# Optimization experiments

Measured on AMD Instinct MI355X. Metric: run time of the kernel, lower is better.

## Reference

```python
import jax, jax.numpy as jnp
import numpy as np
from jax import lax

# Model dims (mamba_ssm defaults: d_state=16, d_conv=4, expand=2, dt_rank=ceil(d_model/16))
V = 16384       # vocab_size
D = 1024        # embedding_dim / d_model
C_CLS = 128     # num_CLS_classes
D_INNER = 2 * D # expand * d_model = 2048
N = 16          # d_state
K = 4           # d_conv
DT_RANK = (D + 15) // 16  # 64
B, L = 4, 512


def setup_inputs() -> dict:
    key = jax.random.key(0)
    ks = jax.random.split(key, 12)
    s = 0.02
    tokens = jax.random.randint(ks[0], (B, L), 0, V, dtype=jnp.int64)
    embedding = jax.random.normal(ks[1], (V, D), jnp.float32) * s
    in_proj_w = jax.random.normal(ks[2], (2 * D_INNER, D), jnp.float32) * s
    conv_w = jax.random.normal(ks[3], (D_INNER, 1, K), jnp.float32) * 0.1
    conv_b = jnp.zeros((D_INNER,), jnp.float32)
    x_proj_w = jax.random.normal(ks[4], (DT_RANK + 2 * N, D_INNER), jnp.float32) * s
    dt_proj_w = jax.random.normal(ks[5], (D_INNER, DT_RANK), jnp.float32) * s
    dt_proj_b = jax.random.uniform(ks[6], (D_INNER,), jnp.float32, -4.0, -2.0)  # softplus -> small dt
    A_log = jnp.log(jnp.broadcast_to(jnp.arange(1, N + 1, dtype=jnp.float32), (D_INNER, N)))
    D_param = jnp.ones((D_INNER,), jnp.float32)
    out_proj_w = jax.random.normal(ks[7], (D, D_INNER), jnp.float32) * s
    recon_w = jax.random.normal(ks[8], (V, D), jnp.float32) * s
    cls_w = jax.random.normal(ks[9], (C_CLS, D), jnp.float32) * s
    return dict(tokens=tokens, embedding=embedding, in_proj_w=in_proj_w,
                conv_w=conv_w, conv_b=conv_b, x_proj_w=x_proj_w,
                dt_proj_w=dt_proj_w, dt_proj_b=dt_proj_b, A_log=A_log,
                D_param=D_param, out_proj_w=out_proj_w, recon_w=recon_w, cls_w=cls_w)


def _mamba(h, in_proj_w, conv_w, conv_b, x_proj_w, dt_proj_w, dt_proj_b, A_log, D_param, out_proj_w):
    # h: (B, L, D)
    xz = jnp.einsum('bld,ed->ble', h, in_proj_w)          # (B, L, 2*D_INNER)
    x, z = jnp.split(xz, 2, axis=-1)                      # each (B, L, D_INNER)
    # causal depthwise conv1d along L
    xt = jnp.swapaxes(x, 1, 2)                            # (B, D_INNER, L)
    xt = lax.conv_general_dilated(xt, conv_w, window_strides=(1,),
                                  padding=[(K - 1, 0)],
                                  feature_group_count=D_INNER,
                                  dimension_numbers=('NCH', 'OIH', 'NCH'))
    xt = xt + conv_b[None, :, None]
    x = jax.nn.silu(jnp.swapaxes(xt, 1, 2))               # (B, L, D_INNER)
    # input-dependent dt, B, C
    x_dbl = jnp.einsum('bld,ed->ble', x, x_proj_w)        # (B, L, DT_RANK+2N)
    dt, Bm, Cm = jnp.split(x_dbl, [DT_RANK, DT_RANK + N], axis=-1)
    delta = jax.nn.softplus(jnp.einsum('blr,dr->bld', dt, dt_proj_w) + dt_proj_b)  # (B,L,D_INNER)
    A = -jnp.exp(A_log)                                   # (D_INNER, N)
    dA = jnp.exp(delta[..., None] * A)                    # (B,L,D_INNER,N)
    dBx = delta[..., None] * Bm[:, :, None, :] * x[..., None]  # (B,L,D_INNER,N)
    # selective scan over time (sequential recurrence)
    dA_t = jnp.swapaxes(dA, 0, 1)                         # (L,B,D_INNER,N)
    dBx_t = jnp.swapaxes(dBx, 0, 1)
    C_t = jnp.swapaxes(Cm, 0, 1)                          # (L,B,N)
    def step(hc, inp):
        a, bx, c = inp
        hc = a * hc + bx                                  # (B,D_INNER,N)
        y = jnp.einsum('bdn,bn->bd', hc, c)
        return hc, y
    h0 = jnp.zeros((x.shape[0], D_INNER, N), x.dtype)
    _, ys = lax.scan(step, h0, (dA_t, dBx_t, C_t))
    y = jnp.swapaxes(ys, 0, 1) + x * D_param              # (B,L,D_INNER)
    y = y * jax.nn.silu(z)
    return jnp.einsum('ble,de->bld', y, out_proj_w)       # (B,L,D)


def reference(tokens, embedding, in_proj_w, conv_w, conv_b, x_proj_w,
              dt_proj_w, dt_proj_b, A_log, D_param, out_proj_w, recon_w, cls_w):
    h = embedding[tokens]                                 # (B,L,D)
    h = _mamba(h, in_proj_w, conv_w, conv_b, x_proj_w, dt_proj_w, dt_proj_b,
               A_log, D_param, out_proj_w)
    recon = jnp.einsum('bld,vd->blv', h, recon_w)         # (B,L,V)
    pooled = h.mean(axis=1)                               # mean CLS pooling assumption
    cls = jnp.einsum('bd,cd->bc', pooled, cls_w)          # (B,C_CLS)
    return (recon, cls)
```

## Files before the change

kernel.cpp:

```cpp
#include <hip/hip_runtime.h>
#include <hip/hip_bf16.h>
#include <stdint.h>

#define DIN    2048
#define MROWS  2048
#define LSEQ   512
#define NV     16384
#define DMODEL 1024
#define NC     8
#define CL     64

typedef __attribute__((ext_vector_type(8))) short bf16x8;
typedef __attribute__((ext_vector_type(4))) float f32x4;

__device__ __forceinline__ uint16_t f2bf(float f) {
  uint32_t u = __builtin_bit_cast(uint32_t, f);
  u += 0x7fffu + ((u >> 16) & 1u);
  return (uint16_t)(u >> 16);
}

__device__ __forceinline__ void gld_lds16(const uint16_t* g, uint16_t* l) {
  __builtin_amdgcn_global_load_lds(
      (const __attribute__((address_space(1))) void*)g,
      (__attribute__((address_space(3))) void*)l,
      16, 0, 0);
}

__global__ __launch_bounds__(512, 2) void gemm256_bf16_kernel(
    const uint16_t* __restrict__ A, const uint16_t* __restrict__ B,
    float* __restrict__ C, int M, int N, int K)
{
  __shared__ uint16_t lds[4 * 16384];
  const int tid = threadIdx.x;
  const int w   = tid >> 6;
  const int l   = tid & 63;

  const int nwg = gridDim.x;
  const int cpx = nwg >> 3;
  const int swz = (blockIdx.x & 7) * cpx + (blockIdx.x >> 3);
  const int nmy = M >> 8;
  const int bm  = (swz % nmy) << 8;
  const int bn  = (swz / nmy) << 8;

  const int fr = l & 15;
  const int fg = l >> 4;
  const int wr = w >> 2;
  const int wc = w & 3;

  const int srow = l >> 2;
  const int kof  = (((l & 3) ^ ((l >> 3) & 3)) << 3);
  const int ar0  = (w * 2 + 0) * 16 + srow;
  const int ar1  = (w * 2 + 1) * 16 + srow;
  const uint16_t* Ag0 = A + (size_t)(bm + ar0) * K + kof;
  const uint16_t* Ag1 = A + (size_t)(bm + ar1) * K + kof;
  const uint16_t* Bg0 = B + (size_t)(bn + ar0) * K + kof;
  const uint16_t* Bg1 = B + (size_t)(bn + ar1) * K + kof;
  const int lA0 = (w * 2 + 0) * 512;
  const int lA1 = (w * 2 + 1) * 512;
  const int lB0 = 8192 + (w * 2 + 0) * 512;
  const int lB1 = 8192 + (w * 2 + 1) * 512;

  const int axr  = ((fg ^ ((fr >> 1) & 3)) << 3);
  const int aoff = (wr * 128 + fr) * 32 + axr;
  const int boff = 8192 + (wc * 64 + fr) * 32 + axr;

  f32x4 acc[8][4] = {};
  const int NT = K >> 5;

  auto stage = [&](int t) {
    const int sb = (t & 3) << 14;
    const int k0 = t << 5;
    gld_lds16(Ag0 + k0, lds + sb + lA0);
    gld_lds16(Ag1 + k0, lds + sb + lA1);
    gld_lds16(Bg0 + k0, lds + sb + lB0);
    gld_lds16(Bg1 + k0, lds + sb + lB1);
  };
  auto compute_tile = [&](int sb) {
    bf16x8 af[8], bfr[4];
#pragma unroll
    for (int mi = 0; mi < 8; ++mi)
      af[mi] = *(const bf16x8*)(lds + sb + aoff + mi * 512);
#pragma unroll
    for (int ni = 0; ni < 4; ++ni)
      bfr[ni] = *(const bf16x8*)(lds + sb + boff + ni * 512);
    __builtin_amdgcn_s_setprio(1);
#pragma unroll
    for (int mi = 0; mi < 8; ++mi)
#pragma unroll
      for (int ni = 0; ni < 4; ++ni)
        acc[mi][ni] = __builtin_amdgcn_mfma_f32_16x16x32_bf16(af[mi], bfr[ni], acc[mi][ni], 0, 0, 0);
    __builtin_amdgcn_s_setprio(0);
  };

  stage(0); stage(1); stage(2);
  asm volatile("s_waitcnt vmcnt(8)" ::: "memory");
  __builtin_amdgcn_s_barrier();

  for (int t = 0; t < NT - 3; ++t) {
    stage(t + 3);
    compute_tile((t & 3) << 14);
    asm volatile("s_waitcnt vmcnt(8)" ::: "memory");
    __builtin_amdgcn_s_barrier();
  }
  compute_tile(((NT - 3) & 3) << 14);
  asm volatile("s_waitcnt vmcnt(4)" ::: "memory");
  __builtin_amdgcn_s_barrier();
  compute_tile(((NT - 2) & 3) << 14);
  asm volatile("s_waitcnt vmcnt(0)" ::: "memory");
  __builtin_amdgcn_s_barrier();
  compute_tile(((NT - 1) & 3) << 14);

#pragma unroll
  for (int mi = 0; mi < 8; ++mi) {
    const int r0 = bm + wr * 128 + mi * 16 + fg * 4;
#pragma unroll
    for (int ni = 0; ni < 4; ++ni) {
      const int c0 = bn + wc * 64 + ni * 16 + fr;
#pragma unroll
      for (int r = 0; r < 4; ++r)
        C[(size_t)(r0 + r) * N + c0] = acc[mi][ni][r];
    }
  }
}

__global__ __launch_bounds__(256) void gemm_bf16_kernel(
    const uint16_t* __restrict__ A, const uint16_t* __restrict__ B,
    float* __restrict__ C, int M, int N, int K, int kchunk)
{
  __shared__ uint16_t As[128 * 32];
  __shared__ uint16_t Bs[128 * 32];
  const int tid  = threadIdx.x;
  const int wid  = tid >> 6;
  const int lane = tid & 63;
  const int bm = blockIdx.y * 128;
  const int bn = blockIdx.x * 128;
  const int k_beg = blockIdx.z * kchunk;
  float* Cout = C + (size_t)blockIdx.z * M * N;

  const int fr = lane & 15;
  const int fg = lane >> 4;
  const int wm = (wid >> 1) * 64;
  const int wn = (wid & 1) * 64;

  const int srow = wid * 32 + (lane >> 2);
  const int skof = (lane & 3) * 8;
  const uint16_t* Ag = A + (size_t)(bm + srow) * K + skof;
  const uint16_t* Bg = B + (size_t)(bn + srow) * K + skof;
  uint16_t* Al = As + wid * 1024;
  uint16_t* Bl = Bs + wid * 1024;

  f32x4 acc[4][4] = {};

  for (int k0 = 0; k0 < kchunk; k0 += 32) {
    const int kk = k_beg + k0;
    gld_lds16(Ag + kk, Al);
    gld_lds16(Ag + (size_t)16 * K + kk, Al + 512);
    gld_lds16(Bg + kk, Bl);
    gld_lds16(Bg + (size_t)16 * K + kk, Bl + 512);
    asm volatile("s_waitcnt vmcnt(0)" ::: "memory");
    __syncthreads();
    bf16x8 af[4], bfr[4];
#pragma unroll
    for (int i = 0; i < 4; ++i)
      af[i] = *(const bf16x8*)(As + (wm + i * 16 + fr) * 32 + fg * 8);
#pragma unroll
    for (int j = 0; j < 4; ++j)
      bfr[j] = *(const bf16x8*)(Bs + (wn + j * 16 + fr) * 32 + fg * 8);
#pragma unroll
    for (int i = 0; i < 4; ++i)
#pragma unroll
      for (int j = 0; j < 4; ++j)
        acc[i][j] = __builtin_amdgcn_mfma_f32_16x16x32_bf16(af[i], bfr[j], acc[i][j], 0, 0, 0);
    __syncthreads();
  }

#pragma unroll
  for (int i = 0; i < 4; ++i) {
    const int r0 = bm + wm + i * 16 + fg * 4;
#pragma unroll
    for (int j = 0; j < 4; ++j) {
      const int c0 = bn + wn + j * 16 + fr;
#pragma unroll
      for (int r = 0; r < 4; ++r)
        Cout[(size_t)(r0 + r) * N + c0] = acc[i][j][r];
    }
  }
}

__global__ __launch_bounds__(256) void reduce_slices_kernel(
    const float* __restrict__ in, float* __restrict__ out, int n, int S) {
  const int i = blockIdx.x * 256 + threadIdx.x;
  if (i >= n) return;
  float s = 0.f;
  for (int z = 0; z < S; ++z) s += in[i + (size_t)z * n];
  out[i] = s;
}

__global__ __launch_bounds__(256) void embed_kernel(
    const int* __restrict__ tok, const float* __restrict__ emb, uint16_t* __restrict__ out) {
  const int m = blockIdx.x;
  const int t = tok[m];
  const float4 v = ((const float4*)(emb + (size_t)t * DMODEL))[threadIdx.x];
  ((ushort4*)(out + (size_t)m * DMODEL))[threadIdx.x] =
      make_ushort4(f2bf(v.x), f2bf(v.y), f2bf(v.z), f2bf(v.w));
}

__global__ __launch_bounds__(256) void cvt_bf16_kernel(
    const float* __restrict__ in, uint16_t* __restrict__ out, int n4) {
  const int i = blockIdx.x * 256 + threadIdx.x;
  if (i >= n4) return;
  const float4 v = ((const float4*)in)[i];
  ((ushort4*)out)[i] = make_ushort4(f2bf(v.x), f2bf(v.y), f2bf(v.z), f2bf(v.w));
}

__global__ __launch_bounds__(256) void cvt_pad_kernel(
    const float* __restrict__ in, uint16_t* __restrict__ out, int rows_in, int cols4) {
  const int i = blockIdx.x * 256 + threadIdx.x;
  const int r = i / cols4, c = i % cols4;
  ushort4 o = make_ushort4(0, 0, 0, 0);
  if (r < rows_in) {
    const float4 v = ((const float4*)in)[(size_t)r * cols4 + c];
    o = make_ushort4(f2bf(v.x), f2bf(v.y), f2bf(v.z), f2bf(v.w));
  }
  ((ushort4*)out)[i] = o;
}

__global__ __launch_bounds__(256) void conv_silu_kernel(
    const float* __restrict__ xz, const float* __restrict__ cw, const float* __restrict__ cb,
    float* __restrict__ xc, uint16_t* __restrict__ xcb)
{
  const int idx = blockIdx.x * 256 + threadIdx.x;
  const int d = idx & (DIN - 1);
  const int m = idx >> 11;
  const int l = m & (LSEQ - 1);
  float acc = cb[d];
#pragma unroll
  for (int j = 0; j < 4; ++j) {
    const int lj = l - 3 + j;
    if (lj >= 0) acc += cw[d * 4 + j] * xz[(size_t)(m - 3 + j) * 4096 + d];
  }
  const float r = acc / (1.f + __expf(-acc));
  xc[idx] = r;
  xcb[idx] = f2bf(r);
}

__global__ __launch_bounds__(256) void dt_extract_kernel(
    const float* __restrict__ xdbl, uint16_t* __restrict__ dtb) {
  const int i = blockIdx.x * 256 + threadIdx.x;
  const int m = i >> 6, r = i & 63;
  dtb[i] = f2bf(xdbl[(size_t)m * 128 + r]);
}

__global__ __launch_bounds__(256) void softplus_kernel(
    float* __restrict__ dlt, const float* __restrict__ bias) {
  const int i = blockIdx.x * 256 + threadIdx.x;
  const int d = i & (DIN - 1);
  const float u = dlt[i] + bias[d];
  dlt[i] = (u > 20.f) ? u : log1pf(__expf(u));
}

__global__ __launch_bounds__(256) void scan_partial_kernel(
    const float* __restrict__ delta, const float* __restrict__ xc,
    const float* __restrict__ xdbl, const float* __restrict__ A_log,
    float* __restrict__ Pb, float* __restrict__ Qb)
{
  const int q = threadIdx.x & 3;
  const int d_idx = threadIdx.x >> 2;
  const int c = blockIdx.x;
  const int d = blockIdx.y * 64 + d_idx;
  const int b = blockIdx.z;
  float Arow[4];
#pragma unroll
  for (int n = 0; n < 4; ++n)
    Arow[n] = -expf(A_log[d * 16 + q * 4 + n]);
  float P[4] = {1.f, 1.f, 1.f, 1.f};
  float Q[4] = {0.f, 0.f, 0.f, 0.f};
  const int l0 = c * CL;
#pragma unroll 4
  for (int li = 0; li < CL; ++li) {
    const int m = b * LSEQ + l0 + li;
    const float de = delta[(size_t)m * DIN + d];
    const float xv = xc[(size_t)m * DIN + d];
    const float dx = de * xv;
    const float4 Bv = *(const float4*)(xdbl + (size_t)m * 128 + 64 + q * 4);
    const float bv[4] = {Bv.x, Bv.y, Bv.z, Bv.w};
#pragma unroll
    for (int n = 0; n < 4; ++n) {
      const float a = __expf(de * Arow[n]);
      P[n] *= a;
      Q[n] = a * Q[n] + dx * bv[n];
    }
  }
  const size_t o = ((size_t)(b * NC + c) * DIN + d) * 16 + q * 4;
  *(float4*)(Pb + o) = make_float4(P[0], P[1], P[2], P[3]);
  *(float4*)(Qb + o) = make_float4(Q[0], Q[1], Q[2], Q[3]);
}

__global__ __launch_bounds__(256) void scan_bounds_kernel(
    const float* __restrict__ Pb, const float* __restrict__ Qb, float* __restrict__ Hi)
{
  const int i = blockIdx.x * 256 + threadIdx.x;
  const int b = i >> 15;
  const int r = i & 32767;
  float h = 0.f;
#pragma unroll
  for (int c = 0; c < NC; ++c) {
    const size_t o = ((size_t)(b * NC + c) << 15) + r;
    Hi[o] = h;
    h = Pb[o] * h + Qb[o];
  }
}

__global__ __launch_bounds__(256) void scan_final_kernel(
    const float* __restrict__ delta, const float* __restrict__ xc,
    const float* __restrict__ xdbl, const float* __restrict__ xz,
    const float* __restrict__ A_log, const float* __restrict__ Dp,
    const float* __restrict__ Hi, uint16_t* __restrict__ yb)
{
  const int q = threadIdx.x & 3;
  const int d_idx = threadIdx.x >> 2;
  const int c = blockIdx.x;
  const int d = blockIdx.y * 64 + d_idx;
  const int b = blockIdx.z;
  float Arow[4];
#pragma unroll
  for (int n = 0; n < 4; ++n)
    Arow[n] = -expf(A_log[d * 16 + q * 4 + n]);
  const float dpd = Dp[d];
  const size_t o = ((size_t)(b * NC + c) * DIN + d) * 16 + q * 4;
  const float4 Hv = *(const float4*)(Hi + o);
  float h[4] = {Hv.x, Hv.y, Hv.z, Hv.w};
  const int l0 = c * CL;
#pragma unroll 2
  for (int li = 0; li < CL; ++li) {
    const int m = b * LSEQ + l0 + li;
    const float de = delta[(size_t)m * DIN + d];
    const float xv = xc[(size_t)m * DIN + d];
    const float dx = de * xv;
    const float4 Bv = *(const float4*)(xdbl + (size_t)m * 128 + 64 + q * 4);
    const float4 Cv = *(const float4*)(xdbl + (size_t)m * 128 + 80 + q * 4);
    const float bv[4] = {Bv.x, Bv.y, Bv.z, Bv.w};
    const float cv[4] = {Cv.x, Cv.y, Cv.z, Cv.w};
    float yp = 0.f;
#pragma unroll
    for (int n = 0; n < 4; ++n) {
      const float a = __expf(de * Arow[n]);
      h[n] = a * h[n] + dx * bv[n];
      yp += h[n] * cv[n];
    }
    yp += __shfl_xor(yp, 1);
    yp += __shfl_xor(yp, 2);
    if (q == 0) {
      const float z = xz[(size_t)m * 4096 + 2048 + d];
      const float sil = z / (1.f + __expf(-z));
      yb[(size_t)m * DIN + d] = f2bf((yp + xv * dpd) * sil);
    }
  }
}

__global__ __launch_bounds__(256) void pool_kernel(
    const float* __restrict__ h2, float* __restrict__ pooled) {
  const int b = blockIdx.x, t = threadIdx.x;
  const float4* base = (const float4*)(h2 + (size_t)b * LSEQ * DMODEL);
  float sx = 0, sy = 0, sz = 0, sw = 0;
  for (int l = 0; l < LSEQ; ++l) {
    const float4 v = base[l * (DMODEL / 4) + t];
    sx += v.x; sy += v.y; sz += v.z; sw += v.w;
  }
  const float inv = 1.f / LSEQ;
  ((float4*)pooled)[b * (DMODEL / 4) + t] = make_float4(sx * inv, sy * inv, sz * inv, sw * inv);
}

__global__ __launch_bounds__(64) void cls_kernel(
    const float* __restrict__ pooled, const float* __restrict__ w, float* __restrict__ out) {
  const int o = blockIdx.x;
  const int b = o >> 7, c = o & 127;
  const int lane = threadIdx.x;
  const float* p = pooled + b * 1024;
  const float* wr = w + c * 1024;
  float s = 0.f;
  for (int k = lane; k < 1024; k += 64) s += p[k] * wr[k];
#pragma unroll
  for (int off = 32; off > 0; off >>= 1) s += __shfl_down(s, off);
  if (lane == 0) out[o] = s;
}

extern "C" void kernel_launch(void* const* d_in, const int* in_sizes, int n_in,
                              void* d_out, int out_size, void* d_ws, size_t ws_size,
                              hipStream_t stream) {
  const int*   tokens    = (const int*)d_in[0];
  const float* embedding = (const float*)d_in[1];
  const float* in_proj_w = (const float*)d_in[2];
  const float* conv_w    = (const float*)d_in[3];
  const float* conv_b    = (const float*)d_in[4];
  const float* x_proj_w  = (const float*)d_in[5];
  const float* dt_proj_w = (const float*)d_in[6];
  const float* dt_proj_b = (const float*)d_in[7];
  const float* A_log     = (const float*)d_in[8];
  const float* D_param   = (const float*)d_in[9];
  const float* out_prj_w = (const float*)d_in[10];
  const float* recon_w   = (const float*)d_in[11];
  const float* cls_w     = (const float*)d_in[12];

  char* ws = (char*)d_ws;
  const size_t MB = 1024 * 1024;
  uint16_t* h_bf   = (uint16_t*)(ws + 0);
  uint16_t* w_in   = (uint16_t*)(ws + 4 * MB);
  float*    xz     = (float*)(ws + 12 * MB);
  float*    xc_f   = (float*)(ws + 44 * MB);
  uint16_t* xc_b   = (uint16_t*)(ws + 60 * MB);
  uint16_t* wx_bf  = (uint16_t*)(ws + 68 * MB);
  float*    xdbl   = (float*)(ws + 69 * MB);
  uint16_t* dt_bf  = (uint16_t*)(ws + 70 * MB);
  uint16_t* wdt_bf = (uint16_t*)(ws + 71 * MB);
  float*    delta  = (float*)(ws + 72 * MB);
  uint16_t* y_bf   = (uint16_t*)(ws + 88 * MB);
  uint16_t* h2_bf  = (uint16_t*)(ws + 96 * MB);
  float*    pooled = (float*)(ws + 100 * MB);
  uint16_t* wout_bf = h_bf;
  float*    h2_f    = (float*)w_in;
  uint16_t* wrec_bf = (uint16_t*)xz;
  float*    kscr    = delta;
  float*    Pbuf    = (float*)(ws + 60 * MB);
  float*    Qbuf    = (float*)(ws + 64 * MB);
  float*    Hinit   = (float*)(ws + 4 * MB);

  const int RECON = MROWS * NV;

  embed_kernel<<<dim3(MROWS), dim3(256), 0, stream>>>(tokens, embedding, h_bf);
  cvt_bf16_kernel<<<dim3(4096), dim3(256), 0, stream>>>(in_proj_w, w_in, 4096 * 1024 / 4);
  gemm256_bf16_kernel<<<dim3(128), dim3(512), 0, stream>>>(h_bf, w_in, xz, MROWS, 4096, 1024);
  cvt_bf16_kernel<<<dim3(2048), dim3(256), 0, stream>>>(out_prj_w, wout_bf, 1024 * 2048 / 4);
  cvt_bf16_kernel<<<dim3(128), dim3(256), 0, stream>>>(dt_proj_w, wdt_bf, 2048 * 64 / 4);
  cvt_pad_kernel<<<dim3(256), dim3(256), 0, stream>>>(x_proj_w, wx_bf, 96, 512);
  conv_silu_kernel<<<dim3(16384), dim3(256), 0, stream>>>(xz, conv_w, conv_b, xc_f, xc_b);
  gemm_bf16_kernel<<<dim3(1, 16, 4), dim3(256), 0, stream>>>(xc_b, wx_bf, kscr, MROWS, 128, 2048, 512);
  reduce_slices_kernel<<<dim3(1024), dim3(256), 0, stream>>>(kscr, xdbl, MROWS * 128, 4);
  dt_extract_kernel<<<dim3(512), dim3(256), 0, stream>>>(xdbl, dt_bf);
  gemm_bf16_kernel<<<dim3(16, 16, 1), dim3(256), 0, stream>>>(dt_bf, wdt_bf, delta, MROWS, DIN, 64, 64);
  softplus_kernel<<<dim3(16384), dim3(256), 0, stream>>>(delta, dt_proj_b);
  scan_partial_kernel<<<dim3(NC, 32, 4), dim3(256), 0, stream>>>(delta, xc_f, xdbl, A_log, Pbuf, Qbuf);
  scan_bounds_kernel<<<dim3(512), dim3(256), 0, stream>>>(Pbuf, Qbuf, Hinit);
  scan_final_kernel<<<dim3(NC, 32, 4), dim3(256), 0, stream>>>(delta, xc_f, xdbl, xz, A_log, D_param, Hinit, y_bf);
  cvt_bf16_kernel<<<dim3(16384), dim3(256), 0, stream>>>(recon_w, wrec_bf, NV * 1024 / 4);
  gemm256_bf16_kernel<<<dim3(32), dim3(512), 0, stream>>>(y_bf, wout_bf, h2_f, MROWS, 1024, 2048);
  cvt_bf16_kernel<<<dim3(2048), dim3(256), 0, stream>>>(h2_f, h2_bf, MROWS * 1024 / 4);
  gemm256_bf16_kernel<<<dim3(512), dim3(512), 0, stream>>>(h2_bf, wrec_bf, (float*)d_out, MROWS, NV, 1024);
  pool_kernel<<<dim3(4), dim3(256), 0, stream>>>(h2_f, pooled);
  cls_kernel<<<dim3(512), dim3(64), 0, stream>>>(pooled, cls_w, (float*)d_out + RECON);
}
```

Baseline: 382.9 us.

## Split GEMM main loop into half-tile phases and fuse small epilogue kernels

Restructures the 256-tile GEMM main loop so A and B loads for the next stage are issued in two halves interleaved with two half-MFMA phases under extra barriers. Softplus is fused into the dt GEMM epilogue, and the split-K reduction is fused with dt extraction. out_proj now uses split-K on the 128-tile GEMM with a reduce that writes bf16 directly. Pooling is done from bf16 h2 in two stages with the classifier fused in. This removes several launches and fp32 round trips, but adds extra barriers in the hot GEMM loop and pools over bf16-rounded values.

```diff
diff --git a/kernel.cpp b/kernel.cpp
--- a/kernel.cpp
+++ b/kernel.cpp
@@ -18,6 +18,9 @@
   u += 0x7fffu + ((u >> 16) & 1u);
   return (uint16_t)(u >> 16);
 }
+__device__ __forceinline__ float bf2f(uint16_t u) {
+  return __builtin_bit_cast(float, (uint32_t)u << 16);
+}
 
 __device__ __forceinline__ void gld_lds16(const uint16_t* g, uint16_t* l) {
   __builtin_amdgcn_global_load_lds(
@@ -28,7 +31,7 @@
 
 __global__ __launch_bounds__(512, 2) void gemm256_bf16_kernel(
     const uint16_t* __restrict__ A, const uint16_t* __restrict__ B,
-    float* __restrict__ C, int M, int N, int K)
+    float* __restrict__ Cf, uint16_t* __restrict__ Cbf, int M, int N, int K)
 {
   __shared__ uint16_t lds[4 * 16384];
   const int tid = threadIdx.x;
@@ -67,7 +70,7 @@
   f32x4 acc[8][4] = {};
   const int NT = K >> 5;
 
-  auto stage = [&](int t) {
+  auto stage_all = [&](int t) {
     const int sb = (t & 3) << 14;
     const int k0 = t << 5;
     gld_lds16(Ag0 + k0, lds + sb + lA0);
@@ -75,7 +78,7 @@
     gld_lds16(Bg0 + k0, lds + sb + lB0);
     gld_lds16(Bg1 + k0, lds + sb + lB1);
   };
-  auto compute_tile = [&](int sb) {
+  auto compute_full = [&](int sb) {
     bf16x8 af[8], bfr[4];
 #pragma unroll
     for (int mi = 0; mi < 8; ++mi)
@@ -92,23 +95,57 @@
     __builtin_amdgcn_s_setprio(0);
   };
 
-  stage(0); stage(1); stage(2);
+  stage_all(0); stage_all(1); stage_all(2);
   asm volatile("s_waitcnt vmcnt(8)" ::: "memory");
   __builtin_amdgcn_s_barrier();
 
   for (int t = 0; t < NT - 3; ++t) {
-    stage(t + 3);
-    compute_tile((t & 3) << 14);
+    const int sb = (t & 3) << 14;
+    const int st = ((t + 3) & 3) << 14;
+    const int k0 = (t + 3) << 5;
+    bf16x8 af[8], bfr[4];
+#pragma unroll
+    for (int mi = 0; mi < 8; ++mi)
+      af[mi] = *(const bf16x8*)(lds + sb + aoff + mi * 512);
+    bfr[0] = *(const bf16x8*)(lds + sb + boff + 0 * 512);
+    bfr[1] = *(const bf16x8*)(lds + sb + boff + 1 * 512);
+    gld_lds16(Ag0 + k0, lds + st + lA0);
+    gld_lds16(Ag1 + k0, lds + st + lA1);
+    __builtin_amdgcn_s_barrier();
+    asm volatile("s_waitcnt lgkmcnt(0)" ::: "memory");
+    __builtin_amdgcn_sched_barrier(0);
+    __builtin_amdgcn_s_setprio(1);
+#pragma unroll
+    for (int mi = 0; mi < 8; ++mi)
+#pragma unroll
+      for (int ni = 0; ni < 2; ++ni)
+        acc[mi][ni] = __builtin_amdgcn_mfma_f32_16x16x32_bf16(af[mi], bfr[ni], acc[mi][ni], 0, 0, 0);
+    __builtin_amdgcn_s_setprio(0);
+    __builtin_amdgcn_s_barrier();
+    bfr[2] = *(const bf16x8*)(lds + sb + boff + 2 * 512);
+    bfr[3] = *(const bf16x8*)(lds + sb + boff + 3 * 512);
+    gld_lds16(Bg0 + k0, lds + st + lB0);
+    gld_lds16(Bg1 + k0, lds + st + lB1);
+    __builtin_amdgcn_s_barrier();
+    asm volatile("s_waitcnt lgkmcnt(0)" ::: "memory");
+    __builtin_amdgcn_sched_barrier(0);
+    __builtin_amdgcn_s_setprio(1);
+#pragma unroll
+    for (int mi = 0; mi < 8; ++mi)
+#pragma unroll
+      for (int ni = 2; ni < 4; ++ni)
+        acc[mi][ni] = __builtin_amdgcn_mfma_f32_16x16x32_bf16(af[mi], bfr[ni], acc[mi][ni], 0, 0, 0);
+    __builtin_amdgcn_s_setprio(0);
     asm volatile("s_waitcnt vmcnt(8)" ::: "memory");
     __builtin_amdgcn_s_barrier();
   }
-  compute_tile(((NT - 3) & 3) << 14);
+  compute_full(((NT - 3) & 3) << 14);
   asm volatile("s_waitcnt vmcnt(4)" ::: "memory");
   __builtin_amdgcn_s_barrier();
-  compute_tile(((NT - 2) & 3) << 14);
+  compute_full(((NT - 2) & 3) << 14);
   asm volatile("s_waitcnt vmcnt(0)" ::: "memory");
   __builtin_amdgcn_s_barrier();
-  compute_tile(((NT - 1) & 3) << 14);
+  compute_full(((NT - 1) & 3) << 14);
 
 #pragma unroll
   for (int mi = 0; mi < 8; ++mi) {
@@ -117,15 +154,19 @@
     for (int ni = 0; ni < 4; ++ni) {
       const int c0 = bn + wc * 64 + ni * 16 + fr;
 #pragma unroll
-      for (int r = 0; r < 4; ++r)
-        C[(size_t)(r0 + r) * N + c0] = acc[mi][ni][r];
+      for (int r = 0; r < 4; ++r) {
+        const float v = acc[mi][ni][r];
+        if (Cf)  Cf[(size_t)(r0 + r) * N + c0] = v;
+        if (Cbf) Cbf[(size_t)(r0 + r) * N + c0] = f2bf(v);
+      }
     }
   }
 }
 
 __global__ __launch_bounds__(256) void gemm_bf16_kernel(
     const uint16_t* __restrict__ A, const uint16_t* __restrict__ B,
-    float* __restrict__ C, int M, int N, int K, int kchunk)
+    float* __restrict__ C, int M, int N, int K, int kchunk,
+    const float* __restrict__ bias)
 {
   __shared__ uint16_t As[128 * 32];
   __shared__ uint16_t Bs[128 * 32];
@@ -180,20 +221,34 @@
 #pragma unroll
     for (int j = 0; j < 4; ++j) {
       const int c0 = bn + wn + j * 16 + fr;
-#pragma unroll
-      for (int r = 0; r < 4; ++r)
-        Cout[(size_t)(r0 + r) * N + c0] = acc[i][j][r];
+      const float bv = bias ? bias[c0] : 0.f;
+#pragma unroll
+      for (int r = 0; r < 4; ++r) {
+        float v = acc[i][j][r];
+        if (bias) {
+          const float u = v + bv;
+          v = (u > 20.f) ? u : log1pf(__expf(u));
+        }
+        Cout[(size_t)(r0 + r) * N + c0] = v;
+      }
     }
   }
 }
 
-__global__ __launch_bounds__(256) void reduce_slices_kernel(
-    const float* __restrict__ in, float* __restrict__ out, int n, int S) {
+__global__ __launch_bounds__(256) void reduce4_dt_kernel(
+    const float* __restrict__ in, float* __restrict__ xdbl, uint16_t* __restrict__ dtb) {
+  const int i = blockIdx.x * 256 + threadIdx.x;
+  const float s = in[i] + in[i + 262144] + in[i + 2 * 262144] + in[i + 3 * 262144];
+  xdbl[i] = s;
+  const int c = i & 127;
+  if (c < 64) dtb[(i >> 7) * 64 + c] = f2bf(s);
+}
+
+__global__ __launch_bounds__(256) void reduce2_bf16_kernel(
+    const float* __restrict__ in, uint16_t* __restrict__ outb, int n) {
   const int i = blockIdx.x * 256 + threadIdx.x;
   if (i >= n) return;
-  float s = 0.f;
-  for (int z = 0; z < S; ++z) s += in[i + (size_t)z * n];
-  out[i] = s;
+  outb[i] = f2bf(in[i] + in[i + (size_t)n]);
 }
 
 __global__ __launch_bounds__(256) void embed_kernel(
@@ -242,21 +297,6 @@
   const float r = acc / (1.f + __expf(-acc));
   xc[idx] = r;
   xcb[idx] = f2bf(r);
-}
-
-__global__ __launch_bounds__(256) void dt_extract_kernel(
-    const float* __restrict__ xdbl, uint16_t* __restrict__ dtb) {
-  const int i = blockIdx.x * 256 + threadIdx.x;
-  const int m = i >> 6, r = i & 63;
-  dtb[i] = f2bf(xdbl[(size_t)m * 128 + r]);
-}
-
-__global__ __launch_bounds__(256) void softplus_kernel(
-    float* __restrict__ dlt, const float* __restrict__ bias) {
-  const int i = blockIdx.x * 256 + threadIdx.x;
-  const int d = i & (DIN - 1);
-  const float u = dlt[i] + bias[d];
-  dlt[i] = (u > 20.f) ? u : log1pf(__expf(u));
 }
 
 __global__ __launch_bounds__(256) void scan_partial_kernel(
@@ -358,31 +398,38 @@
   }
 }
 
-__global__ __launch_bounds__(256) void pool_kernel(
-    const float* __restrict__ h2, float* __restrict__ pooled) {
+__global__ __launch_bounds__(256) void pool1_kernel(
+    const uint16_t* __restrict__ h2b, float* __restrict__ part) {
+  const int b = blockIdx.x >> 4, s = blockIdx.x & 15;
+  const int c = threadIdx.x * 4;
+  const uint16_t* base = h2b + ((size_t)(b * LSEQ + s * 32)) * DMODEL + c;
+  float a0 = 0, a1 = 0, a2 = 0, a3 = 0;
+  for (int l = 0; l < 32; ++l) {
+    const ushort4 v = *(const ushort4*)(base + (size_t)l * DMODEL);
+    a0 += bf2f(v.x); a1 += bf2f(v.y); a2 += bf2f(v.z); a3 += bf2f(v.w);
+  }
+  *(float4*)(part + (size_t)blockIdx.x * DMODEL + c) = make_float4(a0, a1, a2, a3);
+}
+
+__global__ __launch_bounds__(256) void pool2_cls_kernel(
+    const float* __restrict__ part, const float* __restrict__ w, float* __restrict__ out) {
+  __shared__ float pl[DMODEL];
   const int b = blockIdx.x, t = threadIdx.x;
-  const float4* base = (const float4*)(h2 + (size_t)b * LSEQ * DMODEL);
-  float sx = 0, sy = 0, sz = 0, sw = 0;
-  for (int l = 0; l < LSEQ; ++l) {
-    const float4 v = base[l * (DMODEL / 4) + t];
-    sx += v.x; sy += v.y; sz += v.z; sw += v.w;
-  }
-  const float inv = 1.f / LSEQ;
-  ((float4*)pooled)[b * (DMODEL / 4) + t] = make_float4(sx * inv, sy * inv, sz * inv, sw * inv);
-}
-
-__global__ __launch_bounds__(64) void cls_kernel(
-    const float* __restrict__ pooled, const float* __restrict__ w, float* __restrict__ out) {
-  const int o = blockIdx.x;
-  const int b = o >> 7, c = o & 127;
-  const int lane = threadIdx.x;
-  const float* p = pooled + b * 1024;
-  const float* wr = w + c * 1024;
-  float s = 0.f;
-  for (int k = lane; k < 1024; k += 64) s += p[k] * wr[k];
-#pragma unroll
-  for (int off = 32; off > 0; off >>= 1) s += __shfl_down(s, off);
-  if (lane == 0) out[o] = s;
+  float4 s = make_float4(0, 0, 0, 0);
+  for (int k = 0; k < 16; ++k) {
+    const float4 v = *(const float4*)(part + ((size_t)(b * 16 + k)) * DMODEL + t * 4);
+    s.x += v.x; s.y += v.y; s.z += v.z; s.w += v.w;
+  }
+  const float inv = 1.f / (float)LSEQ;
+  pl[t * 4 + 0] = s.x * inv; pl[t * 4 + 1] = s.y * inv;
+  pl[t * 4 + 2] = s.z * inv; pl[t * 4 + 3] = s.w * inv;
+  __syncthreads();
+  if (t < 128) {
+    const float* wr = w + (size_t)t * DMODEL;
+    float acc = 0.f;
+    for (int k = 0; k < DMODEL; ++k) acc += pl[k] * wr[k];
+    out[b * 128 + t] = acc;
+  }
 }
 
 extern "C" void kernel_launch(void* const* d_in, const int* in_sizes, int n_in,
@@ -416,9 +463,8 @@
   float*    delta  = (float*)(ws + 72 * MB);
   uint16_t* y_bf   = (uint16_t*)(ws + 88 * MB);
   uint16_t* h2_bf  = (uint16_t*)(ws + 96 * MB);
-  float*    pooled = (float*)(ws + 100 * MB);
+  float*    part   = (float*)(ws + 100 * MB);
   uint16_t* wout_bf = h_bf;
-  float*    h2_f    = (float*)w_in;
   uint16_t* wrec_bf = (uint16_t*)xz;
   float*    kscr    = delta;
   float*    Pbuf    = (float*)(ws + 60 * MB);
@@ -429,23 +475,21 @@
 
   embed_kernel<<<dim3(MROWS), dim3(256), 0, stream>>>(tokens, embedding, h_bf);
   cvt_bf16_kernel<<<dim3(4096), dim3(256), 0, stream>>>(in_proj_w, w_in, 4096 * 1024 / 4);
-  gemm256_bf16_kernel<<<dim3(128), dim3(512), 0, stream>>>(h_bf, w_in, xz, MROWS, 4096, 1024);
+  gemm256_bf16_kernel<<<dim3(128), dim3(512), 0, stream>>>(h_bf, w_in, xz, nullptr, MROWS, 4096, 1024);
   cvt_bf16_kernel<<<dim3(2048), dim3(256), 0, stream>>>(out_prj_w, wout_bf, 1024 * 2048 / 4);
   cvt_bf16_kernel<<<dim3(128), dim3(256), 0, stream>>>(dt_proj_w, wdt_bf, 2048 * 64 / 4);
   cvt_pad_kernel<<<dim3(256), dim3(256), 0, stream>>>(x_proj_w, wx_bf, 96, 512);
   conv_silu_kernel<<<dim3(16384), dim3(256), 0, stream>>>(xz, conv_w, conv_b, xc_f, xc_b);
-  gemm_bf16_kernel<<<dim3(1, 16, 4), dim3(256), 0, stream>>>(xc_b, wx_bf, kscr, MROWS, 128, 2048, 512);
-  reduce_slices_kernel<<<dim3(1024), dim3(256), 0, stream>>>(kscr, xdbl, MROWS * 128, 4);
-  dt_extract_kernel<<<dim3(512), dim3(256), 0, stream>>>(xdbl, dt_bf);
-  gemm_bf16_kernel<<<dim3(16, 16, 1), dim3(256), 0, stream>>>(dt_bf, wdt_bf, delta, MROWS, DIN, 64, 64);
-  softplus_kernel<<<dim3(16384), dim3(256), 0, stream>>>(delta, dt_proj_b);
+  gemm_bf16_kernel<<<dim3(1, 16, 4), dim3(256), 0, stream>>>(xc_b, wx_bf, kscr, MROWS, 128, 2048, 512, nullptr);
+  reduce4_dt_kernel<<<dim3(1024), dim3(256), 0, stream>>>(kscr, xdbl, dt_bf);
+  gemm_bf16_kernel<<<dim3(16, 16, 1), dim3(256), 0, stream>>>(dt_bf, wdt_bf, delta, MROWS, DIN, 64, 64, dt_proj_b);
   scan_partial_kernel<<<dim3(NC, 32, 4), dim3(256), 0, stream>>>(delta, xc_f, xdbl, A_log, Pbuf, Qbuf);
   scan_bounds_kernel<<<dim3(512), dim3(256), 0, stream>>>(Pbuf, Qbuf, Hinit);
   scan_final_kernel<<<dim3(NC, 32, 4), dim3(256), 0, stream>>>(delta, xc_f, xdbl, xz, A_log, D_param, Hinit, y_bf);
   cvt_bf16_kernel<<<dim3(16384), dim3(256), 0, stream>>>(recon_w, wrec_bf, NV * 1024 / 4);
-  gemm256_bf16_kernel<<<dim3(32), dim3(512), 0, stream>>>(y_bf, wout_bf, h2_f, MROWS, 1024, 2048);
-  cvt_bf16_kernel<<<dim3(2048), dim3(256), 0, stream>>>(h2_f, h2_bf, MROWS * 1024 / 4);
-  gemm256_bf16_kernel<<<dim3(512), dim3(512), 0, stream>>>(h2_bf, wrec_bf, (float*)d_out, MROWS, NV, 1024);
-  pool_kernel<<<dim3(4), dim3(256), 0, stream>>>(h2_f, pooled);
-  cls_kernel<<<dim3(512), dim3(64), 0, stream>>>(pooled, cls_w, (float*)d_out + RECON);
-}
+  gemm_bf16_kernel<<<dim3(8, 16, 2), dim3(256), 0, stream>>>(y_bf, wout_bf, kscr, MROWS, 1024, 2048, 1024, nullptr);
+  reduce2_bf16_kernel<<<dim3(8192), dim3(256), 0, stream>>>(kscr, h2_bf, MROWS * 1024);
+  gemm256_bf16_kernel<<<dim3(512), dim3(512), 0, stream>>>(h2_bf, wrec_bf, (float*)d_out, nullptr, MROWS, NV, 1024);
+  pool1_kernel<<<dim3(64), dim3(256), 0, stream>>>(h2_bf, part);
+  pool2_cls_kernel<<<dim3(4), dim3(256), 0, stream>>>(part, cls_w, (float*)d_out + RECON);
+}
```

Result: faster. 375.0 us (-2.1%).
